# Optimization experiments

Measured on AMD Instinct MI355X. Metric: run time of the kernel, lower is better.

Reference implementation:

```python
import jax, jax.numpy as jnp
import numpy as np

D_MODEL = 1024
N_HEADS = 16
HEAD_DIM = D_MODEL // N_HEADS
BLOCK_SIZE = 2048
B, T = 4, 2048


def setup_inputs() -> dict:
    key = jax.random.key(0)
    ks = jax.random.split(key, 5)
    s = 0.02
    x = jax.random.normal(ks[0], (B, T, D_MODEL), dtype=jnp.float32)
    W_qkv = jax.random.normal(ks[1], (D_MODEL, 3 * D_MODEL), dtype=jnp.float32) * s
    b_qkv = jnp.zeros((3 * D_MODEL,), dtype=jnp.float32)
    W_proj = jax.random.normal(ks[2], (D_MODEL, D_MODEL), dtype=jnp.float32) * s
    b_proj = jnp.zeros((D_MODEL,), dtype=jnp.float32)
    return {"x": x, "W_qkv": W_qkv, "b_qkv": b_qkv, "W_proj": W_proj, "b_proj": b_proj}


def reference(x, W_qkv, b_qkv, W_proj, b_proj):
    Bsz, Tlen, C = x.shape
    qkv = x @ W_qkv + b_qkv                      # [B,T,3C]
    q, k, v = jnp.split(qkv, 3, axis=2)
    # [B,T,C] -> [B,H,T,hd]
    def heads(t):
        return t.reshape(Bsz, Tlen, N_HEADS, HEAD_DIM).transpose(0, 2, 1, 3)
    q, k, v = heads(q), heads(k), heads(v)
    scale = 1.0 / jnp.sqrt(jnp.asarray(HEAD_DIM, dtype=x.dtype))
    att = jnp.einsum('bhqd,bhkd->bhqk', q, k) * scale   # [B,H,T,T]
    causal = jnp.tril(jnp.ones((Tlen, Tlen), dtype=bool))
    att = jnp.where(causal, att, jnp.asarray(-jnp.inf, dtype=att.dtype))
    att = jax.nn.softmax(att, axis=-1)
    y = jnp.einsum('bhqk,bhkd->bhqd', att, v)            # [B,H,T,hd]
    y = y.transpose(0, 2, 1, 3).reshape(Bsz, Tlen, C)
    return y @ W_proj + b_proj
```

## Files before the change

kernel.cpp:

```cpp
#include <hip/hip_runtime.h>
#include <hip/hip_bf16.h>

#define D_MODEL 1024
#define N_HEADS 16
#define HEAD_DIM 64
#define SEQ_T 2048
#define BATCH 4

#define SL2E 0.18033688011f

typedef short s8v  __attribute__((ext_vector_type(8)));
typedef float f32x4 __attribute__((ext_vector_type(4)));
typedef unsigned long long ull;

static __device__ __forceinline__ unsigned short f2bf(float f) {
  union { float f; unsigned int u; } v; v.f = f;
  unsigned int u = v.u;
  return (unsigned short)((u + 0x7FFF + ((u >> 16) & 1)) >> 16);
}

static __device__ __forceinline__ unsigned int cvtpk_bf16(float lo, float hi) {
  unsigned int r;
  asm("v_cvt_pk_bf16_f32 %0, %1, %2" : "=v"(r) : "v"(lo), "v"(hi));
  return r;
}

#if __has_builtin(__builtin_amdgcn_exp2f)
#define EXP2(x) __builtin_amdgcn_exp2f(x)
#else
#define EXP2(x) exp2f(x)
#endif

static __device__ __forceinline__ void glds16(const void* g, void* l) {
  __builtin_amdgcn_global_load_lds(
      (const __attribute__((address_space(1))) void*)g,
      (__attribute__((address_space(3))) void*)l, 16, 0, 0);
}

#define BARRIER() do { asm volatile("" ::: "memory"); \
                       __builtin_amdgcn_s_barrier();  \
                       asm volatile("" ::: "memory"); } while (0)

template<int MODE>
__global__ __launch_bounds__(512, 2) void gemm_bt_kernel(
    const unsigned short* __restrict__ A, const unsigned short* __restrict__ Bt,
    const float* __restrict__ bias, float* __restrict__ Cout,
    unsigned short* __restrict__ qkb, unsigned short* __restrict__ vT,
    int M, int N, int K)
{
  __shared__ unsigned short As[2][256 * 64];
  __shared__ unsigned short Bs[2][128 * 64];

  const int tid  = threadIdx.x;
  const int lane = tid & 63;
  const int wid  = tid >> 6;
  const int col  = lane & 15;
  const int quad = lane >> 4;
  const int cx   = col & 7;
  const int wr   = wid >> 1;
  const int wc   = wid & 1;
  const int bm0  = blockIdx.y * 256;
  const int bn0  = blockIdx.x * 128;
  const int NT   = K >> 6;

  f32x4 acc[4][4];
  #pragma unroll
  for (int t = 0; t < 4; ++t)
    #pragma unroll
    for (int u = 0; u < 4; ++u) acc[t][u] = (f32x4)0.f;

  auto stageA = [&](int t, int bi, int h) {
    const int k0 = t * 64;
    #pragma unroll
    for (int l = 0; l < 2; ++l) {
      int idx = l * 512 + tid;
      int row = h * 128 + (idx >> 3);
      int gc  = (idx & 7) ^ (row & 7);
      glds16(A + (size_t)(bm0 + row) * K + k0 + gc * 8,
             &As[bi][(h * 1024 + idx) * 8]);
    }
  };
  auto stageB = [&](int t, int bi) {
    const int k0 = t * 64;
    #pragma unroll
    for (int l = 0; l < 2; ++l) {
      int idx = l * 512 + tid;
      int row = idx >> 3;
      int gc  = (idx & 7) ^ (row & 7);
      glds16(Bt + (size_t)(bn0 + row) * K + k0 + gc * 8, &Bs[bi][idx * 8]);
    }
  };

  auto body = [&](int t, int bi) {
    s8v af[4][2], bf[4][2];
    if (t + 1 < NT) stageB(t + 1, bi ^ 1);
    #pragma unroll
    for (int tm = 0; tm < 4; ++tm)
      #pragma unroll
      for (int kh = 0; kh < 2; ++kh)
        af[tm][kh] = *(const s8v*)&As[bi][(wr * 64 + tm * 16 + col) * 64 +
                                          (((kh * 4 + quad) ^ cx) * 8)];
    #pragma unroll
    for (int u = 0; u < 4; ++u)
      #pragma unroll
      for (int kh = 0; kh < 2; ++kh)
        bf[u][kh] = *(const s8v*)&Bs[bi][(wc * 64 + u * 16 + col) * 64 +
                                         (((kh * 4 + quad) ^ cx) * 8)];
    __builtin_amdgcn_s_setprio(1);
    #pragma unroll
    for (int tm = 0; tm < 2; ++tm)
      #pragma unroll
      for (int u = 0; u < 2; ++u)
        #pragma unroll
        for (int kh = 0; kh < 2; ++kh)
          acc[tm][u] = __builtin_amdgcn_mfma_f32_16x16x32_bf16(
              af[tm][kh], bf[u][kh], acc[tm][u], 0, 0, 0);
    __builtin_amdgcn_s_setprio(0);
    asm volatile("s_waitcnt lgkmcnt(0)" ::: "memory");
    __builtin_amdgcn_sched_barrier(0);
    BARRIER();

    if (t + 2 < NT) stageA(t + 2, bi, 0);
    __builtin_amdgcn_s_setprio(1);
    #pragma unroll
    for (int tm = 0; tm < 2; ++tm)
      #pragma unroll
      for (int u = 2; u < 4; ++u)
        #pragma unroll
        for (int kh = 0; kh < 2; ++kh)
          acc[tm][u] = __builtin_amdgcn_mfma_f32_16x16x32_bf16(
              af[tm][kh], bf[u][kh], acc[tm][u], 0, 0, 0);
    __builtin_amdgcn_s_setprio(0);
    BARRIER();

    if (t + 2 < NT) stageA(t + 2, bi, 1);
    __builtin_amdgcn_s_setprio(1);
    #pragma unroll
    for (int tm = 2; tm < 4; ++tm)
      #pragma unroll
      for (int u = 2; u < 4; ++u)
        #pragma unroll
        for (int kh = 0; kh < 2; ++kh)
          acc[tm][u] = __builtin_amdgcn_mfma_f32_16x16x32_bf16(
              af[tm][kh], bf[u][kh], acc[tm][u], 0, 0, 0);
    __builtin_amdgcn_s_setprio(0);
    BARRIER();

    __builtin_amdgcn_s_setprio(1);
    #pragma unroll
    for (int tm = 2; tm < 4; ++tm)
      #pragma unroll
      for (int u = 0; u < 2; ++u)
        #pragma unroll
        for (int kh = 0; kh < 2; ++kh)
          acc[tm][u] = __builtin_amdgcn_mfma_f32_16x16x32_bf16(
              af[tm][kh], bf[u][kh], acc[tm][u], 0, 0, 0);
    __builtin_amdgcn_s_setprio(0);
    if (t + 2 < NT) asm volatile("s_waitcnt vmcnt(4)" ::: "memory");
    else            asm volatile("s_waitcnt vmcnt(0)" ::: "memory");
    BARRIER();
  };

  stageA(0, 0, 0); stageA(0, 0, 1); stageB(0, 0);
  stageA(1, 1, 0); stageA(1, 1, 1);
  asm volatile("s_waitcnt vmcnt(4)" ::: "memory");
  BARRIER();

  for (int t = 0; t < NT; t += 2) {
    body(t, 0);
    body(t + 1, 1);
  }

  float bv[4];
  #pragma unroll
  for (int u = 0; u < 4; ++u) bv[u] = bias[bn0 + wc * 64 + u * 16 + col];

  if (MODE == 1 && bn0 >= 2048) {
    #pragma unroll
    for (int tm = 0; tm < 4; ++tm) {
      int m_base = bm0 + wr * 64 + tm * 16 + quad * 4;
      #pragma unroll
      for (int u = 0; u < 4; ++u) {
        int hd = (bn0 + wc * 64 + u * 16 + col) - 2048;
        size_t bh = (size_t)(bm0 >> 11) * 16 + (hd >> 6);
        ull pk = (ull)f2bf(acc[tm][u][0] + bv[u])
               | ((ull)f2bf(acc[tm][u][1] + bv[u]) << 16)
               | ((ull)f2bf(acc[tm][u][2] + bv[u]) << 32)
               | ((ull)f2bf(acc[tm][u][3] + bv[u]) << 48);
        *(ull*)(vT + (bh * 64 + (hd & 63)) * 2048 + (m_base & 2047)) = pk;
      }
    }
  } else {
    const float sc = (MODE == 1 && bn0 < 1024) ? SL2E : 1.0f;
    #pragma unroll
    for (int tm = 0; tm < 4; ++tm) {
      #pragma unroll
      for (int r = 0; r < 4; ++r) {
        size_t m = bm0 + wr * 64 + tm * 16 + quad * 4 + r;
        #pragma unroll
        for (int u = 0; u < 4; ++u) {
          int n = bn0 + wc * 64 + u * 16 + col;
          float v = acc[tm][u][r] + bv[u];
          if (MODE == 0) Cout[m * N + n] = v;
          else           qkb[m * 2048 + n] = f2bf(v * sc);
        }
      }
    }
  }
}

static __device__ __forceinline__ void transpose_tile(
    const float* __restrict__ W, unsigned short* __restrict__ Wt,
    int K, int N, int n0, int k0)
{
  __shared__ float tile[32][33];
  const int tx = threadIdx.x & 31, ty = threadIdx.x >> 5;
  #pragma unroll
  for (int i = 0; i < 4; ++i)
    tile[ty + i * 8][tx] = W[(size_t)(k0 + ty + i * 8) * N + n0 + tx];
  __syncthreads();
  #pragma unroll
  for (int i = 0; i < 4; ++i)
    Wt[(size_t)(n0 + ty + i * 8) * K + k0 + tx] = f2bf(tile[tx][ty + i * 8]);
}

__global__ __launch_bounds__(256) void prep_kernel(
    const float* __restrict__ x, const float* __restrict__ W_qkv,
    const float* __restrict__ W_proj, ushort4* __restrict__ xb,
    unsigned short* __restrict__ wqt, unsigned short* __restrict__ wpt)
{
  const int bid = blockIdx.x;
  if (bid < 8192) {
    int i = bid * 256 + threadIdx.x;
    float4 v = ((const float4*)x)[i];
    ushort4 o;
    o.x = f2bf(v.x); o.y = f2bf(v.y); o.z = f2bf(v.z); o.w = f2bf(v.w);
    xb[i] = o;
  } else if (bid < 8192 + 3072) {
    int b2 = bid - 8192;
    transpose_tile(W_qkv, wqt, 1024, 3072, (b2 % 96) * 32, (b2 / 96) * 32);
  } else {
    int b3 = bid - 11264;
    transpose_tile(W_proj, wpt, 1024, 1024, (b3 % 32) * 32, (b3 / 32) * 32);
  }
}

#define LPAD 72

__global__ __launch_bounds__(256, 3) void attn_mfma_kernel(
    const unsigned short* __restrict__ qk, const unsigned short* __restrict__ vT,
    unsigned short* __restrict__ y)
{
  __shared__ unsigned short Ks[2][64 * 64];
  __shared__ unsigned short Vs[2][64 * 64];
  __shared__ unsigned short Ps[128][LPAD];

  const int tid  = threadIdx.x;
  const int wave = tid >> 6;
  const int lane = tid & 63;
  const int col  = lane & 15;
  const int quad = lane >> 4;
  const int cx   = col & 7;

  const int bh = blockIdx.x;
  const int b = bh >> 4, h = bh & 15;
  const int qblk = 15 - (int)blockIdx.y;
  const int q0 = qblk * 128;
  const int nk = 2 * qblk + 2;
  const int C2 = 2048;

  const unsigned short* qbase = qk + (size_t)b * SEQ_T * C2 + h * 64;
  const unsigned short* kbase = qbase + 1024;
  const unsigned short* vbase = vT + (size_t)bh * 64 * 2048;

  s8v qf[2][2];
  #pragma unroll
  for (int s = 0; s < 2; ++s)
    #pragma unroll
    for (int c = 0; c < 2; ++c)
      qf[s][c] = *(const s8v*)(qbase +
          (size_t)(q0 + s * 64 + wave * 16 + col) * C2 + c * 32 + quad * 8);

  f32x4 acc[2][4];
  #pragma unroll
  for (int s = 0; s < 2; ++s)
    #pragma unroll
    for (int t = 0; t < 4; ++t) acc[s][t] = (f32x4)0.f;
  float lsum[2] = {0.f, 0.f};

  auto stage = [&](int kt, int bi) {
    const int k0 = kt * 64;
    #pragma unroll
    for (int i = 0; i < 2; ++i) {
      int cid = (i * 4 + wave) * 64 + lane;
      int row = cid >> 3;
      int gc  = (cid & 7) ^ (row & 7);
      glds16(kbase + (size_t)(k0 + row) * C2 + gc * 8, &Ks[bi][cid * 8]);
      glds16(vbase + (size_t)row * 2048 + k0 + gc * 8, &Vs[bi][cid * 8]);
    }
  };

  auto tile_body = [&](int kt, int bi) {
    const int k0 = kt * 64;

    s8v kf[4][2];
    #pragma unroll
    for (int t = 0; t < 4; ++t)
      #pragma unroll
      for (int c = 0; c < 2; ++c)
        kf[t][c] = *(const s8v*)&Ks[bi][(t * 16 + col) * 64 + (((c * 4 + quad) ^ cx) * 8)];

    #pragma unroll
    for (int s = 0; s < 2; ++s) {
      const int qs = q0 + s * 64 + wave * 16;
      if (k0 > qs + 15) continue;

      f32x4 st[4];
      #pragma unroll
      for (int t = 0; t < 4; ++t) st[t] = (f32x4)0.f;
      #pragma unroll
      for (int t = 0; t < 4; ++t)
        #pragma unroll
        for (int c = 0; c < 2; ++c)
          st[t] = __builtin_amdgcn_mfma_f32_16x16x32_bf16(kf[t][c], qf[s][c], st[t], 0, 0, 0);

      const bool diag = (k0 + 63 > qs);
      if (!diag) {
        #pragma unroll
        for (int t = 0; t < 4; ++t) {
          float e0 = EXP2(st[t][0]);
          float e1 = EXP2(st[t][1]);
          float e2 = EXP2(st[t][2]);
          float e3 = EXP2(st[t][3]);
          lsum[s] += (e0 + e1) + (e2 + e3);
          uint2 pk;
          pk.x = cvtpk_bf16(e0, e1);
          pk.y = cvtpk_bf16(e2, e3);
          *(uint2*)&Ps[s * 64 + wave * 16 + col][t * 16 + quad * 4] = pk;
        }
      } else {
        const int qg = qs + col;
        #pragma unroll
        for (int t = 0; t < 4; ++t) {
          uint2 pk;
          if (k0 + t * 16 > qs + 15) {
            pk.x = 0u; pk.y = 0u;
          } else {
            float e[4];
            #pragma unroll
            for (int r = 0; r < 4; ++r) {
              float v = EXP2(st[t][r]);
              if (k0 + t * 16 + quad * 4 + r > qg) v = 0.f;
              e[r] = v;
            }
            lsum[s] += (e[0] + e[1]) + (e[2] + e[3]);
            pk.x = cvtpk_bf16(e[0], e[1]);
            pk.y = cvtpk_bf16(e[2], e[3]);
          }
          *(uint2*)&Ps[s * 64 + wave * 16 + col][t * 16 + quad * 4] = pk;
        }
      }
    }

    s8v vf[4][2];
    #pragma unroll
    for (int t = 0; t < 4; ++t)
      #pragma unroll
      for (int c = 0; c < 2; ++c)
        vf[t][c] = *(const s8v*)&Vs[bi][(t * 16 + col) * 64 + (((c * 4 + quad) ^ cx) * 8)];
    #pragma unroll
    for (int s = 0; s < 2; ++s) {
      const int qs = q0 + s * 64 + wave * 16;
      if (k0 > qs + 15) continue;
      s8v pf[2];
      #pragma unroll
      for (int c = 0; c < 2; ++c)
        pf[c] = *(const s8v*)&Ps[s * 64 + wave * 16 + col][c * 32 + quad * 8];
      #pragma unroll
      for (int t = 0; t < 4; ++t)
        #pragma unroll
        for (int c = 0; c < 2; ++c)
          acc[s][t] = __builtin_amdgcn_mfma_f32_16x16x32_bf16(pf[c], vf[t][c], acc[s][t], 0, 0, 0);
    }
  };

  stage(0, 0);
  for (int kt = 0; kt < nk; kt += 2) {
    __syncthreads();
    if (kt + 1 < nk) stage(kt + 1, 1);
    tile_body(kt, 0);
    if (kt + 1 < nk) {
      __syncthreads();
      if (kt + 2 < nk) stage(kt + 2, 0);
      tile_body(kt + 1, 1);
    }
  }

  #pragma unroll
  for (int s = 0; s < 2; ++s) {
    float v = lsum[s];
    v += __shfl_xor(v, 16);
    v += __shfl_xor(v, 32);
    #pragma unroll
    for (int r = 0; r < 4; ++r) {
      float inv = 1.0f / __shfl(v, quad * 4 + r);
      int q = q0 + s * 64 + wave * 16 + quad * 4 + r;
      unsigned short* yrow = y + (size_t)(b * SEQ_T + q) * D_MODEL + h * 64;
      #pragma unroll
      for (int t = 0; t < 4; ++t)
        yrow[t * 16 + col] = f2bf(acc[s][t][r] * inv);
    }
  }
}

extern "C" void kernel_launch(void* const* d_in, const int* in_sizes, int n_in,
                              void* d_out, int out_size, void* d_ws, size_t ws_size,
                              hipStream_t stream) {
  const float* x      = (const float*)d_in[0];
  const float* W_qkv  = (const float*)d_in[1];
  const float* b_qkv  = (const float*)d_in[2];
  const float* W_proj = (const float*)d_in[3];
  const float* b_proj = (const float*)d_in[4];
  float* out = (float*)d_out;

  const int M  = BATCH * SEQ_T;
  const int C  = D_MODEL;
  const int C3 = 3 * D_MODEL;

  unsigned short* xb  = (unsigned short*)d_ws;
  unsigned short* wqt = xb  + (size_t)M * C;
  unsigned short* wpt = wqt + (size_t)C3 * C;
  unsigned short* qkb = wpt + (size_t)C * C;
  unsigned short* vTb = qkb + (size_t)M * 2 * C;
  unsigned short* yb  = vTb + (size_t)64 * 64 * SEQ_T;

  prep_kernel<<<dim3(8192 + 3072 + 1024), dim3(256), 0, stream>>>(
      x, W_qkv, W_proj, (ushort4*)xb, wqt, wpt);

  gemm_bt_kernel<1><<<dim3(C3 / 128, M / 256), dim3(512), 0, stream>>>(
      xb, wqt, b_qkv, nullptr, qkb, vTb, M, C3, C);

  attn_mfma_kernel<<<dim3(BATCH * N_HEADS, SEQ_T / 128), dim3(256), 0, stream>>>(
      qkb, vTb, yb);

  gemm_bt_kernel<0><<<dim3(C / 128, M / 256), dim3(512), 0, stream>>>(
      yb, wpt, b_proj, out, nullptr, nullptr, M, C, C);
}
```

Measured before the change: 242.4 us.

## Triple-buffer A tiles in GEMM and use one barrier per k-step

The GEMM main loop grows the A shared-memory tile from double to triple buffering. Each k-step now issues the next B tile and the A tile two steps ahead up front, then runs all 32 MFMAs in one block and ends with a single barrier. This replaces the old schedule of four barrier-separated phases that interleaved A staging with MFMA quarters. It aims to cut barrier overhead and give loads more time in flight, at the cost of more LDS (the A buffers grow by a third) and losing the fine-grained interleaving of loads with compute.

```diff
diff --git a/kernel.cpp b/kernel.cpp
--- a/kernel.cpp
+++ b/kernel.cpp
@@ -48,7 +48,7 @@
     unsigned short* __restrict__ qkb, unsigned short* __restrict__ vT,
     int M, int N, int K)
 {
-  __shared__ unsigned short As[2][256 * 64];
+  __shared__ unsigned short As[3][256 * 64];
   __shared__ unsigned short Bs[2][128 * 64];
 
   const int tid  = threadIdx.x;
@@ -69,7 +69,7 @@
     #pragma unroll
     for (int u = 0; u < 4; ++u) acc[t][u] = (f32x4)0.f;
 
-  auto stageA = [&](int t, int bi, int h) {
+  auto stageA = [&](int t, int ai, int h) {
     const int k0 = t * 64;
     #pragma unroll
     for (int l = 0; l < 2; ++l) {
@@ -77,7 +77,7 @@
       int row = h * 128 + (idx >> 3);
       int gc  = (idx & 7) ^ (row & 7);
       glds16(A + (size_t)(bm0 + row) * K + k0 + gc * 8,
-             &As[bi][(h * 1024 + idx) * 8]);
+             &As[ai][(h * 1024 + idx) * 8]);
     }
   };
   auto stageB = [&](int t, int bi) {
@@ -91,84 +91,52 @@
     }
   };
 
-  auto body = [&](int t, int bi) {
+  stageA(0, 0, 0); stageA(0, 0, 1); stageB(0, 0);
+  if (NT > 1) {
+    stageA(1, 1, 0); stageA(1, 1, 1);
+    asm volatile("s_waitcnt vmcnt(4)" ::: "memory");
+  } else {
+    asm volatile("s_waitcnt vmcnt(0)" ::: "memory");
+  }
+  BARRIER();
+
+  int ar = 0;
+  for (int t = 0; t < NT; ++t) {
+    const int br = t & 1;
+    const int a2 = (ar + 2 >= 3) ? ar - 1 : ar + 2;
+
+    if (t + 1 < NT) stageB(t + 1, br ^ 1);
+    if (t + 2 < NT) { stageA(t + 2, a2, 0); stageA(t + 2, a2, 1); }
+
     s8v af[4][2], bf[4][2];
-    if (t + 1 < NT) stageB(t + 1, bi ^ 1);
     #pragma unroll
     for (int tm = 0; tm < 4; ++tm)
       #pragma unroll
       for (int kh = 0; kh < 2; ++kh)
-        af[tm][kh] = *(const s8v*)&As[bi][(wr * 64 + tm * 16 + col) * 64 +
+        af[tm][kh] = *(const s8v*)&As[ar][(wr * 64 + tm * 16 + col) * 64 +
                                           (((kh * 4 + quad) ^ cx) * 8)];
     #pragma unroll
     for (int u = 0; u < 4; ++u)
       #pragma unroll
       for (int kh = 0; kh < 2; ++kh)
-        bf[u][kh] = *(const s8v*)&Bs[bi][(wc * 64 + u * 16 + col) * 64 +
+        bf[u][kh] = *(const s8v*)&Bs[br][(wc * 64 + u * 16 + col) * 64 +
                                          (((kh * 4 + quad) ^ cx) * 8)];
     __builtin_amdgcn_s_setprio(1);
     #pragma unroll
-    for (int tm = 0; tm < 2; ++tm)
-      #pragma unroll
-      for (int u = 0; u < 2; ++u)
+    for (int tm = 0; tm < 4; ++tm)
+      #pragma unroll
+      for (int u = 0; u < 4; ++u)
         #pragma unroll
         for (int kh = 0; kh < 2; ++kh)
           acc[tm][u] = __builtin_amdgcn_mfma_f32_16x16x32_bf16(
               af[tm][kh], bf[u][kh], acc[tm][u], 0, 0, 0);
     __builtin_amdgcn_s_setprio(0);
-    asm volatile("s_waitcnt lgkmcnt(0)" ::: "memory");
-    __builtin_amdgcn_sched_barrier(0);
-    BARRIER();
-
-    if (t + 2 < NT) stageA(t + 2, bi, 0);
-    __builtin_amdgcn_s_setprio(1);
-    #pragma unroll
-    for (int tm = 0; tm < 2; ++tm)
-      #pragma unroll
-      for (int u = 2; u < 4; ++u)
-        #pragma unroll
-        for (int kh = 0; kh < 2; ++kh)
-          acc[tm][u] = __builtin_amdgcn_mfma_f32_16x16x32_bf16(
-              af[tm][kh], bf[u][kh], acc[tm][u], 0, 0, 0);
-    __builtin_amdgcn_s_setprio(0);
-    BARRIER();
-
-    if (t + 2 < NT) stageA(t + 2, bi, 1);
-    __builtin_amdgcn_s_setprio(1);
-    #pragma unroll
-    for (int tm = 2; tm < 4; ++tm)
-      #pragma unroll
-      for (int u = 2; u < 4; ++u)
-        #pragma unroll
-        for (int kh = 0; kh < 2; ++kh)
-          acc[tm][u] = __builtin_amdgcn_mfma_f32_16x16x32_bf16(
-              af[tm][kh], bf[u][kh], acc[tm][u], 0, 0, 0);
-    __builtin_amdgcn_s_setprio(0);
-    BARRIER();
-
-    __builtin_amdgcn_s_setprio(1);
-    #pragma unroll
-    for (int tm = 2; tm < 4; ++tm)
-      #pragma unroll
-      for (int u = 0; u < 2; ++u)
-        #pragma unroll
-        for (int kh = 0; kh < 2; ++kh)
-          acc[tm][u] = __builtin_amdgcn_mfma_f32_16x16x32_bf16(
-              af[tm][kh], bf[u][kh], acc[tm][u], 0, 0, 0);
-    __builtin_amdgcn_s_setprio(0);
+
     if (t + 2 < NT) asm volatile("s_waitcnt vmcnt(4)" ::: "memory");
     else            asm volatile("s_waitcnt vmcnt(0)" ::: "memory");
     BARRIER();
-  };
-
-  stageA(0, 0, 0); stageA(0, 0, 1); stageB(0, 0);
-  stageA(1, 1, 0); stageA(1, 1, 1);
-  asm volatile("s_waitcnt vmcnt(4)" ::: "memory");
-  BARRIER();
-
-  for (int t = 0; t < NT; t += 2) {
-    body(t, 0);
-    body(t + 1, 1);
+
+    ar = (ar + 1 == 3) ? 0 : ar + 1;
   }
 
   float bv[4];
```

New measurement: 247.9 us. +2.3%, slower.
